# Optimization experiments

Measured on AMD Instinct MI355X. Metric: run time of the kernel, lower is better.

Reference implementation:

```python
import jax, jax.numpy as jnp
import numpy as np

TAU = 32.0


def setup_inputs() -> dict:
    key = jax.random.key(0)
    k1, k2, k3, k4, k5 = jax.random.split(key, 5)
    B, IN, E, D, M = 32768, 768, 256, 9, 10
    feature = jax.random.normal(k1, (B, IN), dtype=jnp.float32)
    category = jax.random.randint(k2, (B,), 0, D)  # unused in forward math
    # nn.Linear(input_dim, emb_dim, bias=False) stores weight [emb_dim, input_dim]
    W_topic = jax.random.normal(k3, (E, IN), dtype=jnp.float32) * (1.0 / np.sqrt(IN))
    W_domain = jax.random.normal(k4, (E, IN), dtype=jnp.float32) * (1.0 / np.sqrt(IN))
    memory = jax.random.normal(k5, (D, M, E), dtype=jnp.float32)  # stacked domain memory banks
    return {"feature": feature, "category": category, "W_topic": W_topic,
            "W_domain": W_domain, "memory": memory}


def reference(feature, category, W_topic, W_domain, memory):
    # L2-normalize features along dim 1
    f = feature / jnp.linalg.norm(feature, axis=1, keepdims=True)
    topic = f @ W_topic.T      # [B, E]
    dom = f @ W_domain.T       # [B, E]
    # per-domain memory attention, batched over all D domains at once
    att = jax.nn.softmax(jnp.einsum('be,dme->bdm', topic, memory) * TAU, axis=-1)  # [B, D, M]
    sep = jnp.einsum('bdm,dme->bde', att, memory)                                   # [B, D, E]
    domain_att = jnp.einsum('bde,be->bd', sep, dom)                                 # [B, D]
    return jax.nn.softmax(domain_att * TAU, axis=1)[:, None, :]                     # [B, 1, D]
```

## Files before the change

### kernel.cpp

```cpp
#include <hip/hip_runtime.h>
#include <math.h>

typedef __attribute__((ext_vector_type(8))) short short8;
typedef __attribute__((ext_vector_type(4))) float f32x4;
typedef __attribute__((ext_vector_type(8))) unsigned short u16x8;

#define TAUF 32.0f
#define SB() __builtin_amdgcn_sched_barrier(0)
#define BAR() __builtin_amdgcn_s_barrier()

constexpr int B_LO_OFF = 12288;
constexpr int BUF_SZ   = 24576;
constexpr int CSTR     = 196;

__global__ __launch_bounds__(768) void precompute_pr(
    const float* __restrict__ Wt, const float* __restrict__ Wd,
    const float* __restrict__ mem, unsigned short* __restrict__ PRhi,
    unsigned short* __restrict__ PRlo) {
  int r0 = blockIdx.x * 6, t = threadIdx.x;
  if (r0 >= 180) {
    #pragma unroll
    for (int rr = 0; rr < 6; ++rr) {
      PRhi[(size_t)(r0 + rr) * 768 + t] = 0;
      PRlo[(size_t)(r0 + rr) * 768 + t] = 0;
    }
    return;
  }
  __shared__ float mlds[1536];
  const float* W = (r0 >= 90) ? Wd : Wt;
  int dm0 = (r0 >= 90) ? r0 - 90 : r0;
  for (int i = t; i < 1536; i += 768) mlds[i] = mem[(size_t)dm0 * 256 + i];
  __syncthreads();
  float a[6] = {0.f, 0.f, 0.f, 0.f, 0.f, 0.f};
  #pragma unroll 4
  for (int e = 0; e < 256; ++e) {
    float w = W[(size_t)e * 768 + t];
    #pragma unroll
    for (int rr = 0; rr < 6; ++rr) a[rr] += mlds[rr * 256 + e] * w;
  }
  #pragma unroll
  for (int rr = 0; rr < 6; ++rr) {
    unsigned int bu = __float_as_uint(a[rr]);
    unsigned short hi = (unsigned short)(bu >> 16);
    float hf = __uint_as_float(bu & 0xffff0000u);
    unsigned short lo = (unsigned short)(__float_as_uint(a[rr] - hf) >> 16);
    PRhi[(size_t)(r0 + rr) * 768 + t] = hi;
    PRlo[(size_t)(r0 + rr) * 768 + t] = lo;
  }
}

__global__ __launch_bounds__(512, 2) void fused_mfma(
    const float* __restrict__ feat, const unsigned short* __restrict__ PRhi,
    const unsigned short* __restrict__ PRlo, float* __restrict__ out) {
  __shared__ f32x4 smemv[3136];
  __shared__ float invn[128];
  __shared__ float sarr[576];
  char* smem = (char*)smemv;

  const int t    = threadIdx.x;
  const int lane = t & 63;
  const int wid  = t >> 6;
  const int rg   = wid >> 1;
  const int cg   = wid & 1;
  const int b0   = blockIdx.x * 128;

  const float* gA0 = feat + (size_t)(b0 + rg * 32 + (lane & 15)) * 768 +
                     ((lane >> 4) << 3);
  const float* gA1 = gA0 + 16 * 768;

  const int iid  = wid * 3;
  const int bc   = lane >> 2;
  const int bsw  = (lane & 3) ^ ((bc >> 1) & 3);
  const int bsrc = bc * 1536 + bsw * 16;

  const int bfr = ((lane & 15) << 6) |
                  ((((lane >> 4) ^ (((lane & 15) >> 1) & 3)) & 3) << 4);

  f32x4 acc0[6], acc1[6];
  #pragma unroll
  for (int j = 0; j < 6; ++j) {
    acc0[j] = (f32x4){0.f, 0.f, 0.f, 0.f};
    acc1[j] = (f32x4){0.f, 0.f, 0.f, 0.f};
  }
  float ssq0 = 0.f, ssq1 = 0.f;

  auto issueB = [&](int kt, int bb) {
    #pragma unroll
    for (int u = 0; u < 3; ++u) {
      int i  = iid + u;
      int pl = i >= 12;
      int ch = pl ? i - 12 : i;
      const unsigned short* basep = pl ? PRlo : PRhi;
      const char* gg = (const char*)basep + (size_t)ch * 16 * 1536 +
                       kt * 64 + bsrc;
      char* l = smem + bb * BUF_SZ + (pl ? B_LO_OFF : 0) + ch * 1024 +
                lane * 16;
      __builtin_amdgcn_global_load_lds((const unsigned int*)gg,
                                       (unsigned int*)l, 16, 0, 0);
    }
  };

  float4 Aa0, Aa1, Aa2, Aa3, Ab0, Ab1, Ab2, Ab3;
  auto loadAa = [&](int kt) {
    Aa0 = *(const float4*)(gA0 + kt * 32);
    Aa1 = *(const float4*)(gA0 + kt * 32 + 4);
    Aa2 = *(const float4*)(gA1 + kt * 32);
    Aa3 = *(const float4*)(gA1 + kt * 32 + 4);
  };
  auto loadAb = [&](int kt) {
    Ab0 = *(const float4*)(gA0 + kt * 32);
    Ab1 = *(const float4*)(gA0 + kt * 32 + 4);
    Ab2 = *(const float4*)(gA1 + kt * 32);
    Ab3 = *(const float4*)(gA1 + kt * 32 + 4);
  };

  short8 ah0, al0, ah1, al1;
  auto cvtCore = [&](float4 ra0a, float4 ra0b, float4 ra1a, float4 ra1b) {
    float x0[8] = {ra0a.x, ra0a.y, ra0a.z, ra0a.w,
                   ra0b.x, ra0b.y, ra0b.z, ra0b.w};
    float x1[8] = {ra1a.x, ra1a.y, ra1a.z, ra1a.w,
                   ra1b.x, ra1b.y, ra1b.z, ra1b.w};
    u16x8 h0, l0, h1, l1;
    #pragma unroll
    for (int e = 0; e < 8; ++e) {
      float x = x0[e];
      ssq0 += x * x;
      unsigned int bu = __float_as_uint(x);
      h0[e] = (unsigned short)(bu >> 16);
      l0[e] = (unsigned short)(__float_as_uint(
                  x - __uint_as_float(bu & 0xffff0000u)) >> 16);
      float y = x1[e];
      ssq1 += y * y;
      unsigned int bv = __float_as_uint(y);
      h1[e] = (unsigned short)(bv >> 16);
      l1[e] = (unsigned short)(__float_as_uint(
                  y - __uint_as_float(bv & 0xffff0000u)) >> 16);
    }
    ah0 = (short8)h0; al0 = (short8)l0; ah1 = (short8)h1; al1 = (short8)l1;
  };

  auto domfma = [&](int bb) {
    char* base = smem + bb * BUF_SZ;
    #pragma unroll
    for (int j = 0; j < 6; ++j) {
      int chb = (cg * 6 + j) * 1024;
      short8 bh = *(const short8*)(base + chb + bfr);
      short8 bl = *(const short8*)(base + B_LO_OFF + chb + bfr);
      acc0[j] = __builtin_amdgcn_mfma_f32_16x16x32_bf16(ah0, bh, acc0[j], 0, 0, 0);
      acc0[j] = __builtin_amdgcn_mfma_f32_16x16x32_bf16(al0, bh, acc0[j], 0, 0, 0);
      acc0[j] = __builtin_amdgcn_mfma_f32_16x16x32_bf16(ah0, bl, acc0[j], 0, 0, 0);
      acc1[j] = __builtin_amdgcn_mfma_f32_16x16x32_bf16(ah1, bh, acc1[j], 0, 0, 0);
      acc1[j] = __builtin_amdgcn_mfma_f32_16x16x32_bf16(al1, bh, acc1[j], 0, 0, 0);
      acc1[j] = __builtin_amdgcn_mfma_f32_16x16x32_bf16(ah1, bl, acc1[j], 0, 0, 0);
    }
  };

  issueB(0, 0);
  loadAa(0);
  issueB(1, 1);
  loadAb(1);
  asm volatile("s_waitcnt vmcnt(11)" ::: "memory");
  SB(); BAR();

  for (int kp = 0; kp < 11; ++kp) {
    int kt = 2 * kp;
    cvtCore(Aa0, Aa1, Aa2, Aa3);
    domfma(0);
    SB(); BAR();
    issueB(kt + 2, 0);
    loadAa(kt + 2);
    asm volatile("s_waitcnt vmcnt(11)" ::: "memory");
    SB(); BAR();
    cvtCore(Ab0, Ab1, Ab2, Ab3);
    domfma(1);
    SB(); BAR();
    issueB(kt + 3, 1);
    loadAb(kt + 3);
    asm volatile("s_waitcnt vmcnt(11)" ::: "memory");
    SB(); BAR();
  }
  cvtCore(Aa0, Aa1, Aa2, Aa3);
  domfma(0);
  SB(); BAR();
  asm volatile("s_waitcnt vmcnt(4)" ::: "memory");
  SB(); BAR();
  cvtCore(Ab0, Ab1, Ab2, Ab3);
  domfma(1);

  float v0 = ssq0, v1 = ssq1;
  v0 += __shfl_xor(v0, 16, 64); v0 += __shfl_xor(v0, 32, 64);
  v1 += __shfl_xor(v1, 16, 64); v1 += __shfl_xor(v1, 32, 64);
  if (cg == 0 && lane < 16) {
    invn[rg * 32 + lane]      = rsqrtf(v0);
    invn[rg * 32 + 16 + lane] = rsqrtf(v1);
  }
  __syncthreads();

  float* Clds = (float*)smem;
  for (int ph = 0; ph < 2; ++ph) {
    if ((rg >> 1) == ph) {
      int lrow = (rg & 1) * 32;
      #pragma unroll
      for (int rt = 0; rt < 2; ++rt) {
        int rbase = lrow + rt * 16 + ((lane >> 4) << 2);
        int grow  = ph * 64 + rbase;
        #pragma unroll
        for (int j = 0; j < 6; ++j) {
          int col = cg * 96 + j * 16 + (lane & 15);
          f32x4 v = rt ? acc1[j] : acc0[j];
          #pragma unroll
          for (int jj = 0; jj < 4; ++jj)
            Clds[(rbase + jj) * CSTR + col] = v[jj] * invn[grow + jj];
        }
      }
    }
    __syncthreads();

    for (int pid = t; pid < 576; pid += 512) {
      int row = pid / 9, d = pid - row * 9;
      const float* qp = Clds + row * CSTR + d * 10;
      const float* rp = qp + 90;
      float mx = qp[0];
      #pragma unroll
      for (int m = 1; m < 10; ++m) mx = fmaxf(mx, qp[m]);
      float s = 0.f, val = 0.f;
      #pragma unroll
      for (int m = 0; m < 10; ++m) {
        float e = __expf(TAUF * (qp[m] - mx));
        s += e;
        val += e * rp[m];
      }
      sarr[pid] = val / s;
    }
    __syncthreads();

    if (t < 64) {
      float v2[9];
      #pragma unroll
      for (int d = 0; d < 9; ++d) v2[d] = sarr[t * 9 + d];
      float mx = v2[0];
      #pragma unroll
      for (int d = 1; d < 9; ++d) mx = fmaxf(mx, v2[d]);
      float s = 0.f;
      float e[9];
      #pragma unroll
      for (int d = 0; d < 9; ++d) {
        e[d] = __expf(TAUF * (v2[d] - mx));
        s += e[d];
      }
      float is = 1.f / s;
      #pragma unroll
      for (int d = 0; d < 9; ++d)
        out[(size_t)(b0 + ph * 64 + t) * 9 + d] = e[d] * is;
    }
    __syncthreads();
  }
}

extern "C" void kernel_launch(void* const* d_in, const int* in_sizes, int n_in,
                              void* d_out, int out_size, void* d_ws, size_t ws_size,
                              hipStream_t stream) {
  const float* feat = (const float*)d_in[0];
  const float* Wt  = (const float*)d_in[2];
  const float* Wd  = (const float*)d_in[3];
  const float* mem = (const float*)d_in[4];
  float* outp = (float*)d_out;

  unsigned short* PRhi = (unsigned short*)d_ws;
  unsigned short* PRlo = PRhi + 192 * 768;

  precompute_pr<<<32, 768, 0, stream>>>(Wt, Wd, mem, PRhi, PRlo);
  const int B = in_sizes[1];
  fused_mfma<<<B / 128, 512, 0, stream>>>(feat, PRhi, PRlo, outp);
}
```

Measured before the change: 82.96 us.

## Stage feature tiles into LDS via async global_load_lds with swizzle

```diff
diff --git a/kernel.cpp b/kernel.cpp
--- a/kernel.cpp
+++ b/kernel.cpp
@@ -9,8 +9,10 @@
 #define SB() __builtin_amdgcn_sched_barrier(0)
 #define BAR() __builtin_amdgcn_s_barrier()
 
+constexpr int A_SZ     = 16384;
+constexpr int B_BASE   = 32768;
 constexpr int B_LO_OFF = 12288;
-constexpr int BUF_SZ   = 24576;
+constexpr int B_SZ     = 24576;
 constexpr int CSTR     = 196;
 
 __global__ __launch_bounds__(768) void precompute_pr(
@@ -49,10 +51,10 @@
   }
 }
 
-__global__ __launch_bounds__(512, 2) void fused_mfma(
+__global__ __launch_bounds__(512) void fused_mfma(
     const float* __restrict__ feat, const unsigned short* __restrict__ PRhi,
     const unsigned short* __restrict__ PRlo, float* __restrict__ out) {
-  __shared__ f32x4 smemv[3136];
+  __shared__ f32x4 smemv[5120];
   __shared__ float invn[128];
   __shared__ float sarr[576];
   char* smem = (char*)smemv;
@@ -64,25 +66,25 @@
   const int cg   = wid & 1;
   const int b0   = blockIdx.x * 128;
 
-  const float* gA0 = feat + (size_t)(b0 + rg * 32 + (lane & 15)) * 768 +
-                     ((lane >> 4) << 3);
-  const float* gA1 = gA0 + 16 * 768;
+  const char* featB = (const char*)feat;
+
+  auto issueA = [&](int kt, int bb) {
+    #pragma unroll
+    for (int u = 0; u < 2; ++u) {
+      int G   = (wid * 2 + u) * 64 + lane;
+      int row = G >> 3;
+      int kq  = (G & 7) ^ (row & 7);
+      const char* src = featB + (size_t)(b0 + row) * 3072 + kt * 128 + kq * 16;
+      char* dst = smem + bb * A_SZ + G * 16;
+      __builtin_amdgcn_global_load_lds((const unsigned int*)src,
+                                       (unsigned int*)dst, 16, 0, 0);
+    }
+  };
 
   const int iid  = wid * 3;
   const int bc   = lane >> 2;
   const int bsw  = (lane & 3) ^ ((bc >> 1) & 3);
   const int bsrc = bc * 1536 + bsw * 16;
-
-  const int bfr = ((lane & 15) << 6) |
-                  ((((lane >> 4) ^ (((lane & 15) >> 1) & 3)) & 3) << 4);
-
-  f32x4 acc0[6], acc1[6];
-  #pragma unroll
-  for (int j = 0; j < 6; ++j) {
-    acc0[j] = (f32x4){0.f, 0.f, 0.f, 0.f};
-    acc1[j] = (f32x4){0.f, 0.f, 0.f, 0.f};
-  }
-  float ssq0 = 0.f, ssq1 = 0.f;
 
   auto issueB = [&](int kt, int bb) {
     #pragma unroll
@@ -93,54 +95,55 @@
       const unsigned short* basep = pl ? PRlo : PRhi;
       const char* gg = (const char*)basep + (size_t)ch * 16 * 1536 +
                        kt * 64 + bsrc;
-      char* l = smem + bb * BUF_SZ + (pl ? B_LO_OFF : 0) + ch * 1024 +
+      char* l = smem + B_BASE + bb * B_SZ + (pl ? B_LO_OFF : 0) + ch * 1024 +
                 lane * 16;
       __builtin_amdgcn_global_load_lds((const unsigned int*)gg,
                                        (unsigned int*)l, 16, 0, 0);
     }
   };
 
-  float4 Aa0, Aa1, Aa2, Aa3, Ab0, Ab1, Ab2, Ab3;
-  auto loadAa = [&](int kt) {
-    Aa0 = *(const float4*)(gA0 + kt * 32);
-    Aa1 = *(const float4*)(gA0 + kt * 32 + 4);
-    Aa2 = *(const float4*)(gA1 + kt * 32);
-    Aa3 = *(const float4*)(gA1 + kt * 32 + 4);
-  };
-  auto loadAb = [&](int kt) {
-    Ab0 = *(const float4*)(gA0 + kt * 32);
-    Ab1 = *(const float4*)(gA0 + kt * 32 + 4);
-    Ab2 = *(const float4*)(gA1 + kt * 32);
-    Ab3 = *(const float4*)(gA1 + kt * 32 + 4);
-  };
+  const int bfr = ((lane & 15) << 6) |
+                  ((((lane >> 4) ^ (((lane & 15) >> 1) & 3)) & 3) << 4);
+
+  f32x4 acc0[6], acc1[6];
+  #pragma unroll
+  for (int j = 0; j < 6; ++j) {
+    acc0[j] = (f32x4){0.f, 0.f, 0.f, 0.f};
+    acc1[j] = (f32x4){0.f, 0.f, 0.f, 0.f};
+  }
+  float ssq0 = 0.f, ssq1 = 0.f;
 
   short8 ah0, al0, ah1, al1;
-  auto cvtCore = [&](float4 ra0a, float4 ra0b, float4 ra1a, float4 ra1b) {
-    float x0[8] = {ra0a.x, ra0a.y, ra0a.z, ra0a.w,
-                   ra0b.x, ra0b.y, ra0b.z, ra0b.w};
-    float x1[8] = {ra1a.x, ra1a.y, ra1a.z, ra1a.w,
-                   ra1b.x, ra1b.y, ra1b.z, ra1b.w};
-    u16x8 h0, l0, h1, l1;
-    #pragma unroll
-    for (int e = 0; e < 8; ++e) {
-      float x = x0[e];
-      ssq0 += x * x;
-      unsigned int bu = __float_as_uint(x);
-      h0[e] = (unsigned short)(bu >> 16);
-      l0[e] = (unsigned short)(__float_as_uint(
-                  x - __uint_as_float(bu & 0xffff0000u)) >> 16);
-      float y = x1[e];
-      ssq1 += y * y;
-      unsigned int bv = __float_as_uint(y);
-      h1[e] = (unsigned short)(bv >> 16);
-      l1[e] = (unsigned short)(__float_as_uint(
-                  y - __uint_as_float(bv & 0xffff0000u)) >> 16);
-    }
-    ah0 = (short8)h0; al0 = (short8)l0; ah1 = (short8)h1; al1 = (short8)l1;
+
+  auto readA = [&](int bb) {
+    char* base = smem + bb * A_SZ;
+    const int c = lane >> 4;
+    #pragma unroll
+    for (int rt = 0; rt < 2; ++rt) {
+      int row = rg * 32 + rt * 16 + (lane & 15);
+      int p0  = (2 * c)     ^ (row & 7);
+      int p1  = (2 * c + 1) ^ (row & 7);
+      f32x4 v0 = *(const f32x4*)(base + row * 128 + p0 * 16);
+      f32x4 v1 = *(const f32x4*)(base + row * 128 + p1 * 16);
+      float xs[8] = {v0[0], v0[1], v0[2], v0[3], v1[0], v1[1], v1[2], v1[3]};
+      u16x8 h, l;
+      float ss = 0.f;
+      #pragma unroll
+      for (int e = 0; e < 8; ++e) {
+        float x = xs[e];
+        ss += x * x;
+        unsigned int bu = __float_as_uint(x);
+        h[e] = (unsigned short)(bu >> 16);
+        l[e] = (unsigned short)(__float_as_uint(
+                   x - __uint_as_float(bu & 0xffff0000u)) >> 16);
+      }
+      if (rt == 0) { ah0 = (short8)h; al0 = (short8)l; ssq0 += ss; }
+      else         { ah1 = (short8)h; al1 = (short8)l; ssq1 += ss; }
+    }
   };
 
   auto domfma = [&](int bb) {
-    char* base = smem + bb * BUF_SZ;
+    char* base = smem + B_BASE + bb * B_SZ;
     #pragma unroll
     for (int j = 0; j < 6; ++j) {
       int chb = (cg * 6 + j) * 1024;
@@ -155,36 +158,32 @@
     }
   };
 
-  issueB(0, 0);
-  loadAa(0);
-  issueB(1, 1);
-  loadAb(1);
-  asm volatile("s_waitcnt vmcnt(11)" ::: "memory");
+  issueA(0, 0); issueB(0, 0);
+  issueA(1, 1); issueB(1, 1);
+  asm volatile("s_waitcnt vmcnt(5)" ::: "memory");
   SB(); BAR();
 
   for (int kp = 0; kp < 11; ++kp) {
     int kt = 2 * kp;
-    cvtCore(Aa0, Aa1, Aa2, Aa3);
+    readA(0);
     domfma(0);
     SB(); BAR();
-    issueB(kt + 2, 0);
-    loadAa(kt + 2);
-    asm volatile("s_waitcnt vmcnt(11)" ::: "memory");
-    SB(); BAR();
-    cvtCore(Ab0, Ab1, Ab2, Ab3);
+    issueA(kt + 2, 0); issueB(kt + 2, 0);
+    asm volatile("s_waitcnt vmcnt(5)" ::: "memory");
+    SB(); BAR();
+    readA(1);
     domfma(1);
     SB(); BAR();
-    issueB(kt + 3, 1);
-    loadAb(kt + 3);
-    asm volatile("s_waitcnt vmcnt(11)" ::: "memory");
-    SB(); BAR();
-  }
-  cvtCore(Aa0, Aa1, Aa2, Aa3);
+    issueA(kt + 3, 1); issueB(kt + 3, 1);
+    asm volatile("s_waitcnt vmcnt(5)" ::: "memory");
+    SB(); BAR();
+  }
+  readA(0);
   domfma(0);
   SB(); BAR();
-  asm volatile("s_waitcnt vmcnt(4)" ::: "memory");
+  asm volatile("s_waitcnt vmcnt(0)" ::: "memory");
   SB(); BAR();
-  cvtCore(Ab0, Ab1, Ab2, Ab3);
+  readA(1);
   domfma(1);
 
   float v0 = ssq0, v1 = ssq1;
```

Result: faster. 71.07 us (-14.3%).
